# Optimization experiments

Measured on AMD Instinct MI355X. Metric: run time of the kernel, lower is better.

Reference implementation:

```python
import jax, jax.numpy as jnp
import numpy as np

N = 100000   # nodes
E = 1600000  # edges (before self-loops)
F = 128      # in_dim
C = 32       # hidden_dim
H1 = 2       # heads of gat1
G = 64       # graphs in batch
NEG = 0.2    # leaky_relu slope (PyG default)


def segment_softmax(s, idx, num):
    # softmax of s grouped by idx (PyG `softmax`), s: [E, ...], idx: [E]
    m = jax.ops.segment_max(s, idx, num_segments=num)
    m = jnp.where(jnp.isfinite(m), m, 0.0)  # empty segments -> 0 baseline
    e = jnp.exp(s - m[idx])
    d = jax.ops.segment_sum(e, idx, num_segments=num)
    return e / (d[idx] + 1e-16)


def gatv2_layer(x, src, dst, Wl, bl, Wr, br, att, bias, heads, ch):
    # Faithful PyG GATv2Conv (share_weights=False, concat=True)
    n = x.shape[0]
    xl = (x @ Wl + bl).reshape(n, heads, ch)  # source transform
    xr = (x @ Wr + br).reshape(n, heads, ch)  # target transform
    e = jax.nn.leaky_relu(xl[src] + xr[dst], NEG)       # [E, H, C]
    alpha = jnp.sum(e * att, axis=-1)                    # [E, H]
    alpha = segment_softmax(alpha, dst, n)               # softmax over incoming edges
    out = jax.ops.segment_sum(alpha[..., None] * xl[src], dst, num_segments=n)
    return out.reshape(n, heads * ch) + bias


def setup_inputs() -> dict:
    key = jax.random.key(0)
    ks = jax.random.split(key, 24)
    s = 0.1
    inp = {
        "x": jax.random.normal(ks[0], (N, F), jnp.float32),
        "edge_index": jax.random.randint(ks[1], (2, E), 0, N),
        "batch": jnp.sort(jax.random.randint(ks[2], (N,), 0, G)),
        # gat1: in=F, heads=2, out=C
        "Wl1": jax.random.normal(ks[3], (F, H1 * C), jnp.float32) * s,
        "bl1": jnp.zeros((H1 * C,), jnp.float32),
        "Wr1": jax.random.normal(ks[4], (F, H1 * C), jnp.float32) * s,
        "br1": jnp.zeros((H1 * C,), jnp.float32),
        "att1": jax.random.normal(ks[5], (H1, C), jnp.float32) * s,
        "bias1": jnp.zeros((H1 * C,), jnp.float32),
        # gat2: in=2C, heads=1, out=C
        "Wl2": jax.random.normal(ks[6], (H1 * C, C), jnp.float32) * s,
        "bl2": jnp.zeros((C,), jnp.float32),
        "Wr2": jax.random.normal(ks[7], (H1 * C, C), jnp.float32) * s,
        "br2": jnp.zeros((C,), jnp.float32),
        "att2": jax.random.normal(ks[8], (1, C), jnp.float32) * s,
        "bias2": jnp.zeros((C,), jnp.float32),
        # gate_nn: Linear(C,C) -> ReLU -> Linear(C,1)
        "Wg1": jax.random.normal(ks[9], (C, C), jnp.float32) * s,
        "bg1": jnp.zeros((C,), jnp.float32),
        "Wg2": jax.random.normal(ks[10], (C, 1), jnp.float32) * s,
        "bg2": jnp.zeros((1,), jnp.float32),
        # head
        "W1": jax.random.normal(ks[11], (C, C), jnp.float32) * s,
        "b1": jnp.zeros((C,), jnp.float32),
        "W2": jax.random.normal(ks[12], (C, 1), jnp.float32) * s,
        "b2": jnp.zeros((1,), jnp.float32),
    }
    return inp


def reference(x, edge_index, batch,
              Wl1, bl1, Wr1, br1, att1, bias1,
              Wl2, bl2, Wr2, br2, att2, bias2,
              Wg1, bg1, Wg2, bg2, W1, b1, W2, b2):
    n = x.shape[0]
    ar = jnp.arange(n, dtype=edge_index.dtype)
    ei = jnp.concatenate([edge_index, jnp.stack([ar, ar])], axis=1)  # add self-loops
    src, dst = ei[0], ei[1]
    h = jax.nn.relu(gatv2_layer(x, src, dst, Wl1, bl1, Wr1, br1, att1, bias1, H1, C))
    h = jax.nn.relu(gatv2_layer(h, src, dst, Wl2, bl2, Wr2, br2, att2, bias2, 1, C))
    # GlobalAttention pooling
    gate = jax.nn.relu(h @ Wg1 + bg1) @ Wg2 + bg2   # [N, 1]
    a = segment_softmax(gate, batch, G)              # softmax per graph
    p = jax.ops.segment_sum(a * h, batch, num_segments=G)  # [G, C]
    o = jax.nn.relu(p @ W1 + b1) @ W2 + b2           # [G, 1]
    return o.squeeze(-1)
```

## Files before the change

### kernel.cpp

```cpp
#include <hip/hip_runtime.h>
#include <math.h>


constexpr float NEG_SLOPE = 0.2f;

typedef short bf16x8 __attribute__((ext_vector_type(8)));
typedef float f32x4  __attribute__((ext_vector_type(4)));

#define DPP_ADD(v, ctrl)                                                             \
  do {                                                                               \
    int _t = __builtin_amdgcn_update_dpp(0, __float_as_int(v), (ctrl), 0xF, 0xF, true); \
    (v) = (v) + __int_as_float(_t);                                                  \
  } while (0)
#define REDUCE8(v) do { DPP_ADD(v, 0xB1); DPP_ADD(v, 0x4E); DPP_ADD(v, 0x141); } while (0)

__device__ __forceinline__ unsigned short f2bf(float f) {
  unsigned u = __float_as_uint(f);
  return (unsigned short)((u + 0x7FFFu + ((u >> 16) & 1u)) >> 16);
}
__device__ __forceinline__ float bf2f(unsigned short h) {
  return __uint_as_float(((unsigned)h) << 16);
}

__global__ __launch_bounds__(256) void wtrans_kernel(const float* __restrict__ Wl,
    const float* __restrict__ Wr, unsigned short* __restrict__ WT, int K, int NHALF)
{
  int groups = 2 * NHALF * (K / 8);
  for (int g = blockIdx.x * 256 + threadIdx.x; g < groups; g += gridDim.x * 256) {
    int col = g / (K / 8);
    int kb  = (g % (K / 8)) * 8;
    const float* W = (col < NHALF) ? Wl : Wr;
    int c = (col < NHALF) ? col : col - NHALF;
    float v[8];
#pragma unroll
    for (int i = 0; i < 8; ++i) v[i] = W[(size_t)(kb + i) * NHALF + c];
    ushort4 h0, h1;
    h0.x = f2bf(v[0]); h0.y = f2bf(v[1]); h0.z = f2bf(v[2]); h0.w = f2bf(v[3]);
    h1.x = f2bf(v[4]); h1.y = f2bf(v[5]); h1.z = f2bf(v[6]); h1.w = f2bf(v[7]);
    *(ushort4*)&WT[(size_t)col * K + kb]     = h0;
    *(ushort4*)&WT[(size_t)col * K + kb + 4] = h1;
  }
}

template<int K, int NHALF>
__global__ __launch_bounds__(256) void mm_mfma_kernel(const float* __restrict__ x,
    const unsigned short* __restrict__ WT,
    const float* __restrict__ bl, const float* __restrict__ br,
    unsigned short* __restrict__ outl, float* __restrict__ outr, int n)
{
  constexpr int NC = 2 * NHALF;
  constexpr int NT = NC / 16;
  constexpr int KC = K / 32;
  __shared__ unsigned short xs[64 * K];
  const int t = threadIdx.x;
  const int rowbase = blockIdx.x * 64;

  constexpr int GPT = (64 * K / 8) / 256;
#pragma unroll
  for (int g = 0; g < GPT; ++g) {
    int idx = t + g * 256;
    int row = idx / (K / 8);
    int kb  = (idx % (K / 8)) * 8;
    int grow = rowbase + row;
    float4 a0 = make_float4(0.f, 0.f, 0.f, 0.f), a1 = a0;
    if (grow < n) {
      a0 = *(const float4*)&x[(size_t)grow * K + kb];
      a1 = *(const float4*)&x[(size_t)grow * K + kb + 4];
    }
    ushort4 h0, h1;
    h0.x = f2bf(a0.x); h0.y = f2bf(a0.y); h0.z = f2bf(a0.z); h0.w = f2bf(a0.w);
    h1.x = f2bf(a1.x); h1.y = f2bf(a1.y); h1.z = f2bf(a1.z); h1.w = f2bf(a1.w);
    int ksw = kb ^ ((row & 7) << 3);
    *(ushort4*)&xs[row * K + ksw]     = h0;
    *(ushort4*)&xs[row * K + ksw + 4] = h1;
  }
  __syncthreads();

  const int w = t >> 6, l = t & 63;
  const int arow = w * 16 + (l & 15);
  const int kgrp = (l >> 4) * 8;
  const int asw  = (arow & 7) << 3;

  f32x4 zero = {0.f, 0.f, 0.f, 0.f};
  f32x4 acc[NT];
#pragma unroll
  for (int i = 0; i < NT; ++i) acc[i] = zero;

#pragma unroll
  for (int kc = 0; kc < KC; ++kc) {
    int k0 = kc * 32 + kgrp;
    bf16x8 a = *(const bf16x8*)&xs[arow * K + (k0 ^ asw)];
#pragma unroll
    for (int ct = 0; ct < NT; ++ct) {
      bf16x8 b = *(const bf16x8*)&WT[(size_t)(ct * 16 + (l & 15)) * K + k0];
      acc[ct] = __builtin_amdgcn_mfma_f32_16x16x32_bf16(a, b, acc[ct], 0, 0, 0);
    }
  }

  const int orow0 = rowbase + w * 16 + (l >> 4) * 4;
#pragma unroll
  for (int ct = 0; ct < NT; ++ct) {
    int c = ct * 16 + (l & 15);
    bool isl = c < NHALF;
    float bb = isl ? bl[c] : br[c - NHALF];
#pragma unroll
    for (int j = 0; j < 4; ++j) {
      int row = orow0 + j;
      if (row < n) {
        float v = acc[ct][j] + bb;
        if (isl) outl[(size_t)row * NHALF + c] = f2bf(v);
        else     outr[(size_t)row * NHALF + (c - NHALF)] = v;
      }
    }
  }
}

__global__ __launch_bounds__(256) void gate_kernel(const float* __restrict__ h2,
    const float* __restrict__ Wg1, const float* __restrict__ bg1,
    const float* __restrict__ Wg2, const float* __restrict__ bg2,
    float* __restrict__ gate, int n)
{
  int row = blockIdx.x * 256 + threadIdx.x;
  int rr = (row < n) ? row : 0;
  const float* hp = h2 + (size_t)rr * 32;
  float acc[32];
#pragma unroll
  for (int c = 0; c < 32; ++c) acc[c] = 0.f;
  for (int k0 = 0; k0 < 32; k0 += 8) {
    float4 a0 = *(const float4*)(hp + k0 + 0);
    float4 a1 = *(const float4*)(hp + k0 + 4);
    float xk[8];
    xk[0]=a0.x; xk[1]=a0.y; xk[2]=a0.z; xk[3]=a0.w;
    xk[4]=a1.x; xk[5]=a1.y; xk[6]=a1.z; xk[7]=a1.w;
#pragma unroll
    for (int kk = 0; kk < 8; ++kk) {
      const float* wv = Wg1 + (size_t)(k0 + kk) * 32;
#pragma unroll
      for (int c = 0; c < 32; ++c) acc[c] = fmaf(xk[kk], wv[c], acc[c]);
    }
  }
  if (row < n) {
    float g = 0.f;
#pragma unroll
    for (int c = 0; c < 32; ++c)
      g = fmaf(fmaxf(acc[c] + bg1[c], 0.f), Wg2[c], g);
    gate[row] = g + bg2[0];
  }
}

__global__ __launch_bounds__(256) void bucket_hist_kernel(const int* __restrict__ ei,
    int* __restrict__ buk_cnt, int E, int nbuk)
{
  __shared__ int h[512];
  for (int b = threadIdx.x; b < 512; b += 256) h[b] = 0;
  __syncthreads();
  int total = gridDim.x * 256;
  for (int i = blockIdx.x * 256 + threadIdx.x; i < E; i += total)
    atomicAdd(&h[((unsigned)ei[E + i]) >> 8], 1);
  __syncthreads();
  for (int b = threadIdx.x; b < nbuk; b += 256)
    if (h[b]) atomicAdd(&buk_cnt[b], h[b]);
}

__global__ __launch_bounds__(512) void scan_buckets_kernel(const int* __restrict__ buk_cnt,
    int* __restrict__ sbuk_off, int* __restrict__ buk_run, int nbuk, int E)
{
  __shared__ int lds[512];
  int t = threadIdx.x;
  int v = (t < nbuk) ? buk_cnt[t] : 0;
  lds[t] = v; __syncthreads();
  for (int off = 1; off < 512; off <<= 1) {
    int x = (t >= off) ? lds[t - off] : 0;
    __syncthreads();
    lds[t] += x;
    __syncthreads();
  }
  int excl = lds[t] - v;
  if (t < nbuk) { sbuk_off[t] = excl; buk_run[t] = excl; }
  if (t == nbuk) sbuk_off[t] = E;
}

__global__ __launch_bounds__(256) void partition_kernel(const int* __restrict__ ei,
    int* __restrict__ buk_run, unsigned* __restrict__ scratch, int E, int nbuk)
{
  __shared__ int lcnt[512];
  __shared__ int lbase[512];
  int t = threadIdx.x;
  for (int b = t; b < 512; b += 256) lcnt[b] = 0;
  __syncthreads();
  int chunk = (E + gridDim.x - 1) / gridDim.x;
  int s = blockIdx.x * chunk, e = min(E, s + chunk);
  for (int i = s + t; i < e; i += 256)
    atomicAdd(&lcnt[((unsigned)ei[E + i]) >> 8], 1);
  __syncthreads();
  for (int b = t; b < nbuk; b += 256) {
    int c = lcnt[b];
    lbase[b] = c ? atomicAdd(&buk_run[b], c) : 0;
    lcnt[b] = 0;
  }
  __syncthreads();
  for (int i = s + t; i < e; i += 256) {
    int src = ei[i];
    unsigned d = (unsigned)ei[E + i];
    int b = d >> 8;
    int r = atomicAdd(&lcnt[b], 1);
    scratch[lbase[b] + r] = (unsigned)src | ((d & 255u) << 17);
  }
}

__global__ __launch_bounds__(256) void bucket_fill_kernel(const unsigned* __restrict__ scratch,
    const int* __restrict__ sbuk_off, int* __restrict__ row_ptr,
    int* __restrict__ csr_src, int n, int nbuk)
{
  __shared__ int lcnt[256], sexcl[256], cnt2[256];
  int b = blockIdx.x, t = threadIdx.x;
  int dst0 = b << 8;
  int ndst = min(256, n - dst0);
  int s = sbuk_off[b], e = sbuk_off[b + 1];
  int base = s + dst0;
  lcnt[t] = (t < ndst) ? 1 : 0;
  __syncthreads();
  for (int i = s + t; i < e; i += 256)
    atomicAdd(&lcnt[scratch[i] >> 17], 1);
  __syncthreads();
  int c0 = lcnt[t];
  for (int off = 1; off < 256; off <<= 1) {
    int x = (t >= off) ? lcnt[t - off] : 0;
    __syncthreads();
    lcnt[t] += x;
    __syncthreads();
  }
  int ex = lcnt[t] - c0;
  sexcl[t] = ex;
  cnt2[t] = 1;
  if (t < ndst) {
    row_ptr[dst0 + t] = base + ex;
    csr_src[base + ex] = dst0 + t;
  }
  if (b == nbuk - 1 && t == 0) row_ptr[n] = sbuk_off[nbuk] + n;
  __syncthreads();
  for (int i = s + t; i < e; i += 256) {
    unsigned u = scratch[i];
    int dl = u >> 17;
    int src = u & 0x1FFFF;
    int pos = base + sexcl[dl] + atomicAdd(&cnt2[dl], 1);
    csr_src[pos] = src;
  }
}

__global__ __launch_bounds__(256) void gat1_kernel(const unsigned short* __restrict__ xl,
    const float* __restrict__ xr, const int* __restrict__ row_ptr,
    const int* __restrict__ csr_src, const float* __restrict__ att,
    const float* __restrict__ bias, float* __restrict__ hout, int n)
{
  int wid = (blockIdx.x * 256 + threadIdx.x) >> 6;
  if (wid >= n) return;
  wid = __builtin_amdgcn_readfirstlane(wid);
  int l = threadIdx.x & 63;
  int g = l >> 4;
  int q = l & 15;
  float4 xrv = *(const float4*)&xr[(size_t)wid * 64 + q * 4];
  float4 attv = *(const float4*)&att[q * 4];
  float4 attn = make_float4(attv.x * NEG_SLOPE, attv.y * NEG_SLOPE,
                            attv.z * NEG_SLOPE, attv.w * NEG_SLOPE);
  int s = row_ptr[wid], e = row_ptr[wid + 1];
  float4 accA = make_float4(0.f, 0.f, 0.f, 0.f);
  float4 accB = make_float4(0.f, 0.f, 0.f, 0.f);
  float dA = 0.f, dB = 0.f;
  for (int cb = s; cb < e; cb += 8) {
#define EDGE1(OFF, dS, aS) {                                                  \
    int idx = cb + (OFF) + g;                                                 \
    int src = csr_src[min(idx, e - 1)];                                       \
    ushort4 hv = *(const ushort4*)&xl[(size_t)src * 64 + q * 4];              \
    float4 xlv = make_float4(bf2f(hv.x), bf2f(hv.y), bf2f(hv.z), bf2f(hv.w)); \
    float tx = xlv.x + xrv.x, ty = xlv.y + xrv.y;                             \
    float tz = xlv.z + xrv.z, tw = xlv.w + xrv.w;                             \
    float v =      tx * ((tx > 0.f) ? attv.x : attn.x);                       \
    v = fmaf(ty, ((ty > 0.f) ? attv.y : attn.y), v);                          \
    v = fmaf(tz, ((tz > 0.f) ? attv.z : attn.z), v);                          \
    v = fmaf(tw, ((tw > 0.f) ? attv.w : attn.w), v);                          \
    REDUCE8(v);                                                               \
    float p = __expf(v);                                                      \
    p = (idx < e) ? p : 0.f;                                                  \
    dS += p;                                                                  \
    aS.x = fmaf(p, xlv.x, aS.x);                                              \
    aS.y = fmaf(p, xlv.y, aS.y);                                              \
    aS.z = fmaf(p, xlv.z, aS.z);                                              \
    aS.w = fmaf(p, xlv.w, aS.w); }
    EDGE1(0, dA, accA)
    EDGE1(4, dB, accB)
#undef EDGE1
  }
  float4 acc;
  acc.x = accA.x + accB.x; acc.y = accA.y + accB.y;
  acc.z = accA.z + accB.z; acc.w = accA.w + accB.w;
  float d = dA + dB;
  acc.x += __shfl_xor(acc.x, 16); acc.x += __shfl_xor(acc.x, 32);
  acc.y += __shfl_xor(acc.y, 16); acc.y += __shfl_xor(acc.y, 32);
  acc.z += __shfl_xor(acc.z, 16); acc.z += __shfl_xor(acc.z, 32);
  acc.w += __shfl_xor(acc.w, 16); acc.w += __shfl_xor(acc.w, 32);
  d += __shfl_xor(d, 16); d += __shfl_xor(d, 32);
  if (g == 0) {
    float inv = 1.f / (d + 1e-16f);
    float4 b4 = *(const float4*)&bias[q * 4];
    float4 o;
    o.x = fmaxf(fmaf(acc.x, inv, b4.x), 0.f);
    o.y = fmaxf(fmaf(acc.y, inv, b4.y), 0.f);
    o.z = fmaxf(fmaf(acc.z, inv, b4.z), 0.f);
    o.w = fmaxf(fmaf(acc.w, inv, b4.w), 0.f);
    *(float4*)&hout[(size_t)wid * 64 + q * 4] = o;
  }
}

__global__ __launch_bounds__(256) void gat2_kernel(const unsigned short* __restrict__ xl,
    const float* __restrict__ xr, const int* __restrict__ row_ptr,
    const int* __restrict__ csr_src, const float* __restrict__ att,
    const float* __restrict__ bias, float* __restrict__ hout, int n)
{
  int wid = (blockIdx.x * 256 + threadIdx.x) >> 6;
  if (wid >= n) return;
  wid = __builtin_amdgcn_readfirstlane(wid);
  int l = threadIdx.x & 63;
  int g8 = l >> 3;
  int q = l & 7;
  float4 xrv = *(const float4*)&xr[(size_t)wid * 32 + q * 4];
  float4 attv = *(const float4*)&att[q * 4];
  float4 attn = make_float4(attv.x * NEG_SLOPE, attv.y * NEG_SLOPE,
                            attv.z * NEG_SLOPE, attv.w * NEG_SLOPE);
  int s = row_ptr[wid], e = row_ptr[wid + 1];
  int deg = e - s;
  float4 accA = make_float4(0.f, 0.f, 0.f, 0.f);
  float4 accB = make_float4(0.f, 0.f, 0.f, 0.f);
  float dA = 0.f, dB = 0.f;
  for (int i0 = 0; i0 < deg; i0 += 16) {
#define EDGE2(OFF, dS, aS) {                                                  \
    int ii = i0 + (OFF) + g8;                                                 \
    int src = csr_src[s + min(ii, deg - 1)];                                  \
    ushort4 hv = *(const ushort4*)&xl[(size_t)src * 32 + q * 4];              \
    float4 xlv = make_float4(bf2f(hv.x), bf2f(hv.y), bf2f(hv.z), bf2f(hv.w)); \
    float tx = xlv.x + xrv.x, ty = xlv.y + xrv.y;                             \
    float tz = xlv.z + xrv.z, tw = xlv.w + xrv.w;                             \
    float v =      tx * ((tx > 0.f) ? attv.x : attn.x);                       \
    v = fmaf(ty, ((ty > 0.f) ? attv.y : attn.y), v);                          \
    v = fmaf(tz, ((tz > 0.f) ? attv.z : attn.z), v);                          \
    v = fmaf(tw, ((tw > 0.f) ? attv.w : attn.w), v);                          \
    REDUCE8(v);                                                               \
    float p = __expf(v);                                                      \
    p = (ii < deg) ? p : 0.f;                                                 \
    dS += p;                                                                  \
    aS.x = fmaf(p, xlv.x, aS.x);                                              \
    aS.y = fmaf(p, xlv.y, aS.y);                                              \
    aS.z = fmaf(p, xlv.z, aS.z);                                              \
    aS.w = fmaf(p, xlv.w, aS.w); }
    EDGE2(0, dA, accA)
    EDGE2(8, dB, accB)
#undef EDGE2
  }
  float4 acc;
  acc.x = accA.x + accB.x; acc.y = accA.y + accB.y;
  acc.z = accA.z + accB.z; acc.w = accA.w + accB.w;
  float d = dA + dB;
  acc.x += __shfl_xor(acc.x, 8); acc.x += __shfl_xor(acc.x, 16); acc.x += __shfl_xor(acc.x, 32);
  acc.y += __shfl_xor(acc.y, 8); acc.y += __shfl_xor(acc.y, 16); acc.y += __shfl_xor(acc.y, 32);
  acc.z += __shfl_xor(acc.z, 8); acc.z += __shfl_xor(acc.z, 16); acc.z += __shfl_xor(acc.z, 32);
  acc.w += __shfl_xor(acc.w, 8); acc.w += __shfl_xor(acc.w, 16); acc.w += __shfl_xor(acc.w, 32);
  d += __shfl_xor(d, 8); d += __shfl_xor(d, 16); d += __shfl_xor(d, 32);
  if (g8 == 0) {
    float inv = 1.f / (d + 1e-16f);
    float4 b4 = *(const float4*)&bias[q * 4];
    float4 o;
    o.x = fmaxf(fmaf(acc.x, inv, b4.x), 0.f);
    o.y = fmaxf(fmaf(acc.y, inv, b4.y), 0.f);
    o.z = fmaxf(fmaf(acc.z, inv, b4.z), 0.f);
    o.w = fmaxf(fmaf(acc.w, inv, b4.w), 0.f);
    *(float4*)&hout[(size_t)wid * 32 + q * 4] = o;
  }
}

__global__ __launch_bounds__(1024) void pool_head_kernel(const float* __restrict__ h2,
    const float* __restrict__ gate, const int* __restrict__ batch,
    const float* __restrict__ W1, const float* __restrict__ b1,
    const float* __restrict__ W2, const float* __restrict__ b2,
    float* __restrict__ out, int n)
{
  int g = blockIdx.x;
  int t = threadIdx.x;
  int lo = 0, hi = n;
  while (lo < hi) { int mid = (lo + hi) >> 1; if (batch[mid] < g) lo = mid + 1; else hi = mid; }
  int s = lo;
  lo = s; hi = n;
  while (lo < hi) { int mid = (lo + hi) >> 1; if (batch[mid] < g + 1) lo = mid + 1; else hi = mid; }
  int e = lo;

  __shared__ float red[1024];
  float lm = -INFINITY;
  for (int i = s + t; i < e; i += 1024) lm = fmaxf(lm, gate[i]);
  red[t] = lm; __syncthreads();
  for (int off = 512; off > 0; off >>= 1) {
    if (t < off) red[t] = fmaxf(red[t], red[t + off]);
    __syncthreads();
  }
  float m = (s == e) ? 0.f : red[0];
  __syncthreads();

  int c = t & 31, grp = t >> 5;
  float acc = 0.f, dsum = 0.f;
  for (int i = s + grp; i < e; i += 32) {
    float sv = __expf(gate[i] - m);
    acc += sv * h2[(size_t)i * 32 + c];
    if (c == 0) dsum += sv;
  }
  __shared__ float accs[32][33];
  __shared__ float dss[32];
  accs[grp][c] = acc;
  if (c == 0) dss[grp] = dsum;
  __syncthreads();

  if (t < 32) {
    float a = 0.f, dd = 0.f;
#pragma unroll
    for (int k = 0; k < 32; ++k) { a += accs[k][t]; dd += dss[k]; }
    float p = a / (dd + 1e-16f);
    float q = 0.f;
    for (int cc = 0; cc < 32; ++cc)
      q = fmaf(__shfl(p, cc, 32), W1[cc * 32 + t], q);
    q = fmaxf(q + b1[t], 0.f);
    float r = q * W2[t];
    r += __shfl_xor(r, 1, 32);  r += __shfl_xor(r, 2, 32);
    r += __shfl_xor(r, 4, 32);  r += __shfl_xor(r, 8, 32);
    r += __shfl_xor(r, 16, 32);
    if (t == 0) out[g] = r + b2[0];
  }
}

extern "C" void kernel_launch(void* const* d_in, const int* in_sizes, int n_in,
                              void* d_out, int out_size, void* d_ws, size_t ws_size,
                              hipStream_t stream)
{
  const float* x     = (const float*)d_in[0];
  const int*   ei    = (const int*)d_in[1];
  const int*   batch = (const int*)d_in[2];
  const float* Wl1   = (const float*)d_in[3];
  const float* bl1   = (const float*)d_in[4];
  const float* Wr1   = (const float*)d_in[5];
  const float* br1   = (const float*)d_in[6];
  const float* att1  = (const float*)d_in[7];
  const float* bias1 = (const float*)d_in[8];
  const float* Wl2   = (const float*)d_in[9];
  const float* bl2   = (const float*)d_in[10];
  const float* Wr2   = (const float*)d_in[11];
  const float* br2   = (const float*)d_in[12];
  const float* att2  = (const float*)d_in[13];
  const float* bias2 = (const float*)d_in[14];
  const float* Wg1   = (const float*)d_in[15];
  const float* bg1   = (const float*)d_in[16];
  const float* Wg2   = (const float*)d_in[17];
  const float* bg2   = (const float*)d_in[18];
  const float* W1    = (const float*)d_in[19];
  const float* b1    = (const float*)d_in[20];
  const float* W2    = (const float*)d_in[21];
  const float* b2    = (const float*)d_in[22];
  float* out = (float*)d_out;

  const int n = in_sizes[2];
  const int E = in_sizes[1] / 2;
  const int Etot = E + n;
  const int nbuk = (n + 255) / 256;

  float* fws = (float*)d_ws;
  size_t nf64 = (size_t)n * 64;
  float* bufA = fws;
  float* bufB = bufA + nf64;
  float* bufC = bufB + nf64;
  unsigned short* xl1 = (unsigned short*)bufA;
  float* xr1 = bufB;
  float* hbuf = bufC;
  unsigned short* xl2 = (unsigned short*)bufA;
  float* xr2 = bufA + (size_t)n * 16;
  float* h2  = bufB;
  float* gate = bufB + (size_t)n * 32;
  unsigned* scratch = (unsigned*)bufC;
  int* ip       = (int*)(bufC + nf64);
  int* row_ptr  = ip;  ip += (n + 2);
  int* buk_cnt  = ip;  ip += 512;
  int* sbuk_off = ip;  ip += 520;
  int* buk_run  = ip;  ip += 512;
  int* csr_src  = ip;  ip += Etot;
  unsigned short* WT1 = (unsigned short*)ip;
  unsigned short* WT2 = WT1 + 128 * 128;

  hipMemsetAsync(buk_cnt, 0, 512 * sizeof(int), stream);

  int mb64 = (n + 63) / 64;

  wtrans_kernel<<<8, 256, 0, stream>>>(Wl1, Wr1, WT1, 128, 64);
  wtrans_kernel<<<2, 256, 0, stream>>>(Wl2, Wr2, WT2, 64, 32);

  mm_mfma_kernel<128, 64><<<mb64, 256, 0, stream>>>(x, WT1, bl1, br1, xl1, xr1, n);

  bucket_hist_kernel<<<256, 256, 0, stream>>>(ei, buk_cnt, E, nbuk);
  scan_buckets_kernel<<<1, 512, 0, stream>>>(buk_cnt, sbuk_off, buk_run, nbuk, E);
  partition_kernel<<<256, 256, 0, stream>>>(ei, buk_run, scratch, E, nbuk);
  bucket_fill_kernel<<<nbuk, 256, 0, stream>>>(scratch, sbuk_off, row_ptr, csr_src, n, nbuk);

  int gatblocks = (n + 3) / 4;
  gat1_kernel<<<gatblocks, 256, 0, stream>>>(xl1, xr1, row_ptr, csr_src, att1, bias1, hbuf, n);

  mm_mfma_kernel<64, 32><<<mb64, 256, 0, stream>>>(hbuf, WT2, bl2, br2, xl2, xr2, n);

  gat2_kernel<<<gatblocks, 256, 0, stream>>>(xl2, xr2, row_ptr, csr_src, att2, bias2, h2, n);

  gate_kernel<<<(n + 255) / 256, 256, 0, stream>>>(h2, Wg1, bg1, Wg2, bg2, gate, n);

  pool_head_kernel<<<64, 1024, 0, stream>>>(h2, gate, batch, W1, b1, W2, b2, out, n);
}
```

Before: 263.2 us.

## Widen per-lane edge gathers to 16 bytes and software-prefetch next edge rows

In both GATv2 aggregation kernels, each lane now handles 8 bf16 features with one 16-byte load instead of 4 features with an 8-byte load. More edges are therefore processed per wavefront step: 8 per step in gat1, 16 in gat2. The head-dot reduction shrinks from 8 lanes to 4, and the next iteration's neighbor row is loaded before the current one is computed, to hide gather latency. In exchange the kernels use more registers and need one more cross-lane shuffle stage at the end, and the explicit two-way unroll is replaced by single-step prefetching.

```diff
diff --git a/kernel.cpp b/kernel.cpp
--- a/kernel.cpp
+++ b/kernel.cpp
@@ -12,7 +12,7 @@
     int _t = __builtin_amdgcn_update_dpp(0, __float_as_int(v), (ctrl), 0xF, 0xF, true); \
     (v) = (v) + __int_as_float(_t);                                                  \
   } while (0)
-#define REDUCE8(v) do { DPP_ADD(v, 0xB1); DPP_ADD(v, 0x4E); DPP_ADD(v, 0x141); } while (0)
+#define REDUCE4(v) do { DPP_ADD(v, 0xB1); DPP_ADD(v, 0x4E); } while (0)
 
 __device__ __forceinline__ unsigned short f2bf(float f) {
   unsigned u = __float_as_uint(f);
@@ -21,6 +21,8 @@
 __device__ __forceinline__ float bf2f(unsigned short h) {
   return __uint_as_float(((unsigned)h) << 16);
 }
+__device__ __forceinline__ float bfLO(unsigned u) { return __uint_as_float(u << 16); }
+__device__ __forceinline__ float bfHI(unsigned u) { return __uint_as_float(u & 0xFFFF0000u); }
 
 __global__ __launch_bounds__(256) void wtrans_kernel(const float* __restrict__ Wl,
     const float* __restrict__ Wr, unsigned short* __restrict__ WT, int K, int NHALF)
@@ -257,58 +259,78 @@
   if (wid >= n) return;
   wid = __builtin_amdgcn_readfirstlane(wid);
   int l = threadIdx.x & 63;
-  int g = l >> 4;
-  int q = l & 15;
-  float4 xrv = *(const float4*)&xr[(size_t)wid * 64 + q * 4];
-  float4 attv = *(const float4*)&att[q * 4];
-  float4 attn = make_float4(attv.x * NEG_SLOPE, attv.y * NEG_SLOPE,
-                            attv.z * NEG_SLOPE, attv.w * NEG_SLOPE);
+  int g8 = l >> 3;
+  int q = l & 7;
+  float xrv[8], attv[8], attn[8];
+  {
+    float4 x0 = *(const float4*)&xr[(size_t)wid * 64 + q * 8];
+    float4 x1 = *(const float4*)&xr[(size_t)wid * 64 + q * 8 + 4];
+    float4 a0 = *(const float4*)&att[q * 8];
+    float4 a1 = *(const float4*)&att[q * 8 + 4];
+    xrv[0]=x0.x; xrv[1]=x0.y; xrv[2]=x0.z; xrv[3]=x0.w;
+    xrv[4]=x1.x; xrv[5]=x1.y; xrv[6]=x1.z; xrv[7]=x1.w;
+    attv[0]=a0.x; attv[1]=a0.y; attv[2]=a0.z; attv[3]=a0.w;
+    attv[4]=a1.x; attv[5]=a1.y; attv[6]=a1.z; attv[7]=a1.w;
+#pragma unroll
+    for (int i = 0; i < 8; ++i) attn[i] = attv[i] * NEG_SLOPE;
+  }
   int s = row_ptr[wid], e = row_ptr[wid + 1];
-  float4 accA = make_float4(0.f, 0.f, 0.f, 0.f);
-  float4 accB = make_float4(0.f, 0.f, 0.f, 0.f);
-  float dA = 0.f, dB = 0.f;
+  float acc[8];
+#pragma unroll
+  for (int i = 0; i < 8; ++i) acc[i] = 0.f;
+  float d = 0.f;
+
+#define LOAD1(CB, hv) {                                                       \
+    int src_ = csr_src[min((CB) + g8, e - 1)];                                \
+    hv = *(const int4*)&xl[(size_t)src_ * 64 + q * 8]; }
+
+  int4 cur;
+  LOAD1(s, cur)
   for (int cb = s; cb < e; cb += 8) {
-#define EDGE1(OFF, dS, aS) {                                                  \
-    int idx = cb + (OFF) + g;                                                 \
-    int src = csr_src[min(idx, e - 1)];                                       \
-    ushort4 hv = *(const ushort4*)&xl[(size_t)src * 64 + q * 4];              \
-    float4 xlv = make_float4(bf2f(hv.x), bf2f(hv.y), bf2f(hv.z), bf2f(hv.w)); \
-    float tx = xlv.x + xrv.x, ty = xlv.y + xrv.y;                             \
-    float tz = xlv.z + xrv.z, tw = xlv.w + xrv.w;                             \
-    float v =      tx * ((tx > 0.f) ? attv.x : attn.x);                       \
-    v = fmaf(ty, ((ty > 0.f) ? attv.y : attn.y), v);                          \
-    v = fmaf(tz, ((tz > 0.f) ? attv.z : attn.z), v);                          \
-    v = fmaf(tw, ((tw > 0.f) ? attv.w : attn.w), v);                          \
-    REDUCE8(v);                                                               \
-    float p = __expf(v);                                                      \
-    p = (idx < e) ? p : 0.f;                                                  \
-    dS += p;                                                                  \
-    aS.x = fmaf(p, xlv.x, aS.x);                                              \
-    aS.y = fmaf(p, xlv.y, aS.y);                                              \
-    aS.z = fmaf(p, xlv.z, aS.z);                                              \
-    aS.w = fmaf(p, xlv.w, aS.w); }
-    EDGE1(0, dA, accA)
-    EDGE1(4, dB, accB)
-#undef EDGE1
-  }
-  float4 acc;
-  acc.x = accA.x + accB.x; acc.y = accA.y + accB.y;
-  acc.z = accA.z + accB.z; acc.w = accA.w + accB.w;
-  float d = dA + dB;
-  acc.x += __shfl_xor(acc.x, 16); acc.x += __shfl_xor(acc.x, 32);
-  acc.y += __shfl_xor(acc.y, 16); acc.y += __shfl_xor(acc.y, 32);
-  acc.z += __shfl_xor(acc.z, 16); acc.z += __shfl_xor(acc.z, 32);
-  acc.w += __shfl_xor(acc.w, 16); acc.w += __shfl_xor(acc.w, 32);
-  d += __shfl_xor(d, 16); d += __shfl_xor(d, 32);
-  if (g == 0) {
+    int4 nxt;
+    LOAD1(min(cb + 8, e - 1), nxt)
+    float xc[8];
+    xc[0] = bfLO((unsigned)cur.x); xc[1] = bfHI((unsigned)cur.x);
+    xc[2] = bfLO((unsigned)cur.y); xc[3] = bfHI((unsigned)cur.y);
+    xc[4] = bfLO((unsigned)cur.z); xc[5] = bfHI((unsigned)cur.z);
+    xc[6] = bfLO((unsigned)cur.w); xc[7] = bfHI((unsigned)cur.w);
+    float v = 0.f;
+#pragma unroll
+    for (int i = 0; i < 8; ++i) {
+      float t = xc[i] + xrv[i];
+      v = fmaf(t, (t > 0.f) ? attv[i] : attn[i], v);
+    }
+    REDUCE4(v);
+    float p = __expf(v);
+    p = (cb + g8 < e) ? p : 0.f;
+    d += p;
+#pragma unroll
+    for (int i = 0; i < 8; ++i) acc[i] = fmaf(p, xc[i], acc[i]);
+    cur = nxt;
+  }
+#undef LOAD1
+#pragma unroll
+  for (int i = 0; i < 8; ++i) {
+    acc[i] += __shfl_xor(acc[i], 8);
+    acc[i] += __shfl_xor(acc[i], 16);
+    acc[i] += __shfl_xor(acc[i], 32);
+  }
+  d += __shfl_xor(d, 8); d += __shfl_xor(d, 16); d += __shfl_xor(d, 32);
+  if (g8 == 0) {
     float inv = 1.f / (d + 1e-16f);
-    float4 b4 = *(const float4*)&bias[q * 4];
-    float4 o;
-    o.x = fmaxf(fmaf(acc.x, inv, b4.x), 0.f);
-    o.y = fmaxf(fmaf(acc.y, inv, b4.y), 0.f);
-    o.z = fmaxf(fmaf(acc.z, inv, b4.z), 0.f);
-    o.w = fmaxf(fmaf(acc.w, inv, b4.w), 0.f);
-    *(float4*)&hout[(size_t)wid * 64 + q * 4] = o;
+    float4 b0 = *(const float4*)&bias[q * 8];
+    float4 b1 = *(const float4*)&bias[q * 8 + 4];
+    float4 o0, o1;
+    o0.x = fmaxf(fmaf(acc[0], inv, b0.x), 0.f);
+    o0.y = fmaxf(fmaf(acc[1], inv, b0.y), 0.f);
+    o0.z = fmaxf(fmaf(acc[2], inv, b0.z), 0.f);
+    o0.w = fmaxf(fmaf(acc[3], inv, b0.w), 0.f);
+    o1.x = fmaxf(fmaf(acc[4], inv, b1.x), 0.f);
+    o1.y = fmaxf(fmaf(acc[5], inv, b1.y), 0.f);
+    o1.z = fmaxf(fmaf(acc[6], inv, b1.z), 0.f);
+    o1.w = fmaxf(fmaf(acc[7], inv, b1.w), 0.f);
+    *(float4*)&hout[(size_t)wid * 64 + q * 8]     = o0;
+    *(float4*)&hout[(size_t)wid * 64 + q * 8 + 4] = o1;
   }
 }
 
@@ -321,59 +343,81 @@
   if (wid >= n) return;
   wid = __builtin_amdgcn_readfirstlane(wid);
   int l = threadIdx.x & 63;
-  int g8 = l >> 3;
-  int q = l & 7;
-  float4 xrv = *(const float4*)&xr[(size_t)wid * 32 + q * 4];
-  float4 attv = *(const float4*)&att[q * 4];
-  float4 attn = make_float4(attv.x * NEG_SLOPE, attv.y * NEG_SLOPE,
-                            attv.z * NEG_SLOPE, attv.w * NEG_SLOPE);
+  int g16 = l >> 2;
+  int q = l & 3;
+  float xrv[8], attv[8], attn[8];
+  {
+    float4 x0 = *(const float4*)&xr[(size_t)wid * 32 + q * 8];
+    float4 x1 = *(const float4*)&xr[(size_t)wid * 32 + q * 8 + 4];
+    float4 a0 = *(const float4*)&att[q * 8];
+    float4 a1 = *(const float4*)&att[q * 8 + 4];
+    xrv[0]=x0.x; xrv[1]=x0.y; xrv[2]=x0.z; xrv[3]=x0.w;
+    xrv[4]=x1.x; xrv[5]=x1.y; xrv[6]=x1.z; xrv[7]=x1.w;
+    attv[0]=a0.x; attv[1]=a0.y; attv[2]=a0.z; attv[3]=a0.w;
+    attv[4]=a1.x; attv[5]=a1.y; attv[6]=a1.z; attv[7]=a1.w;
+#pragma unroll
+    for (int i = 0; i < 8; ++i) attn[i] = attv[i] * NEG_SLOPE;
+  }
   int s = row_ptr[wid], e = row_ptr[wid + 1];
   int deg = e - s;
-  float4 accA = make_float4(0.f, 0.f, 0.f, 0.f);
-  float4 accB = make_float4(0.f, 0.f, 0.f, 0.f);
-  float dA = 0.f, dB = 0.f;
+  float acc[8];
+#pragma unroll
+  for (int i = 0; i < 8; ++i) acc[i] = 0.f;
+  float d = 0.f;
+
+#define LOAD2(I0, hv) {                                                       \
+    int src_ = csr_src[s + min((I0) + g16, deg - 1)];                         \
+    hv = *(const int4*)&xl[(size_t)src_ * 32 + q * 8]; }
+
+  int4 cur;
+  LOAD2(0, cur)
   for (int i0 = 0; i0 < deg; i0 += 16) {
-#define EDGE2(OFF, dS, aS) {                                                  \
-    int ii = i0 + (OFF) + g8;                                                 \
-    int src = csr_src[s + min(ii, deg - 1)];                                  \
-    ushort4 hv = *(const ushort4*)&xl[(size_t)src * 32 + q * 4];              \
-    float4 xlv = make_float4(bf2f(hv.x), bf2f(hv.y), bf2f(hv.z), bf2f(hv.w)); \
-    float tx = xlv.x + xrv.x, ty = xlv.y + xrv.y;                             \
-    float tz = xlv.z + xrv.z, tw = xlv.w + xrv.w;                             \
-    float v =      tx * ((tx > 0.f) ? attv.x : attn.x);                       \
-    v = fmaf(ty, ((ty > 0.f) ? attv.y : attn.y), v);                          \
-    v = fmaf(tz, ((tz > 0.f) ? attv.z : attn.z), v);                          \
-    v = fmaf(tw, ((tw > 0.f) ? attv.w : attn.w), v);                          \
-    REDUCE8(v);                                                               \
-    float p = __expf(v);                                                      \
-    p = (ii < deg) ? p : 0.f;                                                 \
-    dS += p;                                                                  \
-    aS.x = fmaf(p, xlv.x, aS.x);                                              \
-    aS.y = fmaf(p, xlv.y, aS.y);                                              \
-    aS.z = fmaf(p, xlv.z, aS.z);                                              \
-    aS.w = fmaf(p, xlv.w, aS.w); }
-    EDGE2(0, dA, accA)
-    EDGE2(8, dB, accB)
-#undef EDGE2
-  }
-  float4 acc;
-  acc.x = accA.x + accB.x; acc.y = accA.y + accB.y;
-  acc.z = accA.z + accB.z; acc.w = accA.w + accB.w;
-  float d = dA + dB;
-  acc.x += __shfl_xor(acc.x, 8); acc.x += __shfl_xor(acc.x, 16); acc.x += __shfl_xor(acc.x, 32);
-  acc.y += __shfl_xor(acc.y, 8); acc.y += __shfl_xor(acc.y, 16); acc.y += __shfl_xor(acc.y, 32);
-  acc.z += __shfl_xor(acc.z, 8); acc.z += __shfl_xor(acc.z, 16); acc.z += __shfl_xor(acc.z, 32);
-  acc.w += __shfl_xor(acc.w, 8); acc.w += __shfl_xor(acc.w, 16); acc.w += __shfl_xor(acc.w, 32);
-  d += __shfl_xor(d, 8); d += __shfl_xor(d, 16); d += __shfl_xor(d, 32);
-  if (g8 == 0) {
+    int4 nxt;
+    LOAD2(min(i0 + 16, deg - 1), nxt)
+    float xc[8];
+    xc[0] = bfLO((unsigned)cur.x); xc[1] = bfHI((unsigned)cur.x);
+    xc[2] = bfLO((unsigned)cur.y); xc[3] = bfHI((unsigned)cur.y);
+    xc[4] = bfLO((unsigned)cur.z); xc[5] = bfHI((unsigned)cur.z);
+    xc[6] = bfLO((unsigned)cur.w); xc[7] = bfHI((unsigned)cur.w);
+    float v = 0.f;
+#pragma unroll
+    for (int i = 0; i < 8; ++i) {
+      float t = xc[i] + xrv[i];
+      v = fmaf(t, (t > 0.f) ? attv[i] : attn[i], v);
+    }
+    REDUCE4(v);
+    float p = __expf(v);
+    p = (i0 + g16 < deg) ? p : 0.f;
+    d += p;
+#pragma unroll
+    for (int i = 0; i < 8; ++i) acc[i] = fmaf(p, xc[i], acc[i]);
+    cur = nxt;
+  }
+#undef LOAD2
+#pragma unroll
+  for (int i = 0; i < 8; ++i) {
+    acc[i] += __shfl_xor(acc[i], 4);
+    acc[i] += __shfl_xor(acc[i], 8);
+    acc[i] += __shfl_xor(acc[i], 16);
+    acc[i] += __shfl_xor(acc[i], 32);
+  }
+  d += __shfl_xor(d, 4); d += __shfl_xor(d, 8);
+  d += __shfl_xor(d, 16); d += __shfl_xor(d, 32);
+  if (g16 == 0) {
     float inv = 1.f / (d + 1e-16f);
-    float4 b4 = *(const float4*)&bias[q * 4];
-    float4 o;
-    o.x = fmaxf(fmaf(acc.x, inv, b4.x), 0.f);
-    o.y = fmaxf(fmaf(acc.y, inv, b4.y), 0.f);
-    o.z = fmaxf(fmaf(acc.z, inv, b4.z), 0.f);
-    o.w = fmaxf(fmaf(acc.w, inv, b4.w), 0.f);
-    *(float4*)&hout[(size_t)wid * 32 + q * 4] = o;
+    float4 b0 = *(const float4*)&bias[q * 8];
+    float4 b1 = *(const float4*)&bias[q * 8 + 4];
+    float4 o0, o1;
+    o0.x = fmaxf(fmaf(acc[0], inv, b0.x), 0.f);
+    o0.y = fmaxf(fmaf(acc[1], inv, b0.y), 0.f);
+    o0.z = fmaxf(fmaf(acc[2], inv, b0.z), 0.f);
+    o0.w = fmaxf(fmaf(acc[3], inv, b0.w), 0.f);
+    o1.x = fmaxf(fmaf(acc[4], inv, b1.x), 0.f);
+    o1.y = fmaxf(fmaf(acc[5], inv, b1.y), 0.f);
+    o1.z = fmaxf(fmaf(acc[6], inv, b1.z), 0.f);
+    o1.w = fmaxf(fmaf(acc[7], inv, b1.w), 0.f);
+    *(float4*)&hout[(size_t)wid * 32 + q * 8]     = o0;
+    *(float4*)&hout[(size_t)wid * 32 + q * 8 + 4] = o1;
   }
 }
 
```

Result: faster. 254.5 us (-3.3%).
